# Kernel tuning notes

Hardware: AMD Instinct MI355X
Metric: run time of the kernel (lower is better)

The kernel has to match this reference:

```python
import jax, jax.numpy as jnp
import numpy as np

# SLAYER SRM-alpha neuron constants (standard slayerPytorch yaml defaults)
THETA = 10.0      # spike threshold
TAU_SR = 10.0     # synaptic response time constant
TAU_REF = 1.0     # refractory time constant
SCALE_REF = 2.0   # refractory scale (kernel amplitude = -scaleRef*theta)
TS = 1.0          # simulation timestep
K_LEN = 100       # SRM kernel truncation length (kernel is negligible beyond this)
A_REF = float(np.exp(-TS / TAU_REF))
# refractory alpha kernel ref[m] = K_REF * m * A_REF**m  (= -scaleRef*theta*(m*Ts/tauRef)*exp(1-m*Ts/tauRef))
K_REF = -SCALE_REF * THETA * float(np.e) * (TS / TAU_REF)


def _srm_kernel():
    # eps(t) = (t/tauSr) * exp(1 - t/tauSr), eps(0) = 0
    t = jnp.arange(K_LEN, dtype=jnp.float32) * TS
    return (t / TAU_SR) * jnp.exp(1.0 - t / TAU_SR)


def _psp(z):
    # z: (N, O, T). Causal FIR convolution in time with the SRM alpha kernel.
    N, O, T = z.shape
    k = _srm_kernel()[::-1].reshape(1, 1, K_LEN)  # flip: lax conv is correlation
    out = jax.lax.conv_general_dilated(z.reshape(N * O, 1, T), k,
                                       window_strides=(1,),
                                       padding=[(K_LEN - 1, 0)])
    return out.reshape(N, O, T)


def _refractory_and_spikes(u):
    # u: (T, N, O) post-synaptic potential. Sequential threshold + alpha refractory.
    # Alpha refractory kernel K*m*a^m is realized as a 2nd-order IIR over spikes:
    #   p[n] = a*p[n-1] + s[n]          (1st-order exp state)
    #   y[n] = a*(y[n-1] + K*p[n-1])    (refractory contribution at step n)
    def step(carry, u_t):
        p, y = carry
        y_n = A_REF * (y + K_REF * p)
        s = (u_t + y_n >= THETA).astype(u_t.dtype) / TS
        return (A_REF * p + s, y_n), (s, y_n)

    z0 = jnp.zeros(u.shape[1:], u.dtype)
    _, (s_seq, y_seq) = jax.lax.scan(step, (z0, z0), u)
    return s_seq, y_seq


def _layer(z):
    # slayer.spike(slayer.psp(fc(x)))
    u = _psp(z)
    s, _ = _refractory_and_spikes(jnp.moveaxis(u, -1, 0))
    return jnp.moveaxis(s, 0, -1)


def setup_inputs():
    key = jax.random.key(0)
    k1, k2, k3 = jax.random.split(key, 3)
    x = (jax.random.uniform(k1, (8, 2, 128, 128, 300)) < 0.03).astype(jnp.float32)
    # weight scales chosen so layer membranes hover around threshold -> realistic spiking
    w1 = jax.random.normal(k2, (410, 2 * 128 * 128), jnp.float32) * 0.01
    w2 = jax.random.normal(k3, (10, 410), jnp.float32) * 0.05
    return {"x": x, "w1": w1, "w2": w2}


def reference(x, w1, w2):
    N, T = x.shape[0], x.shape[-1]
    xf = x.reshape(N, -1, T)  # (N, C*H*W, T): slayer.dense is a full-spatial conv == GEMM per t
    s1 = _layer(jnp.einsum('nit,oi->not', xf, w1))  # fc1 -> psp -> spike, (N, 410, T)
    s2 = _layer(jnp.einsum('nit,oi->not', s1, w2))  # fc2 -> psp -> spike, (N, 10, T)
    return s2
```

## Files before the change

### kernel.cpp

```cpp
#include <hip/hip_runtime.h>

#define N_BATCH 8
#define I_DIM   32768
#define T_DIM   300
#define O1      410
#define O1P     416
#define O1Q     104
#define O2      10
#define KLEN    100
#define NCHUNK  16
#define NWORD   (I_DIM / 32)
#define CHCAP   128
#define NT      (N_BATCH * T_DIM)
#define GRP     4
#define NTG     (NT / GRP)
#define PSTRIDE 308

typedef float nfloat4 __attribute__((ext_vector_type(4)));

__device__ __forceinline__ float4 nt_load4(const float4* p) {
    nfloat4 v = __builtin_nontemporal_load(reinterpret_cast<const nfloat4*>(p));
    return make_float4(v.x, v.y, v.z, v.w);
}
__device__ __forceinline__ void nt_store4(float4* p, float4 v) {
    nfloat4 w = {v.x, v.y, v.z, v.w};
    __builtin_nontemporal_store(w, reinterpret_cast<nfloat4*>(p));
}

__global__ void transpose_w1_k(const float* __restrict__ w1, float* __restrict__ w1t) {
    __shared__ float tile[64][65];
    int i0 = blockIdx.x * 64;
    int o0 = blockIdx.y * 64;
    int tx = threadIdx.x & 63;
    int ty = threadIdx.x >> 6;
#pragma unroll
    for (int r = 0; r < 64; r += 4) {
        int o = o0 + r + ty;
        tile[r + ty][tx] = (o < O1) ? __builtin_nontemporal_load(&w1[(size_t)o * I_DIM + i0 + tx])
                                    : 0.0f;
    }
    __syncthreads();
#pragma unroll
    for (int r = 0; r < 64; r += 4) {
        int i = i0 + r + ty;
        int o = o0 + tx;
        if (o < O1P) w1t[(size_t)i * O1P + o] = (o < O1) ? tile[tx][r + ty] : 0.0f;
    }
}

__global__ __launch_bounds__(256) void bitmask_k(const float* __restrict__ x,
                                                 unsigned int* __restrict__ xb) {
    __shared__ float4 tile4[32 * 75];
    __shared__ unsigned int wbuf[300];
    int w   = blockIdx.x;
    int n   = blockIdx.y;
    int tid = threadIdx.x;
    const float4* src = (const float4*)(x + ((size_t)(n * I_DIM + w * 32)) * T_DIM);
    for (int q = tid; q < 32 * 75; q += 256) tile4[q] = nt_load4(&src[q]);
    __syncthreads();
    const float* tile = (const float*)tile4;
    int wv  = tid >> 6;
    int l   = tid & 63;
    int row = l & 31;
    int th  = l >> 5;
    for (int tp = wv; tp < 150; tp += 4) {
        int t = 2 * tp + th;
        float v = tile[row * 300 + t];
        unsigned long long m = __ballot(v != 0.0f);
        if (l == 0) {
            wbuf[2 * tp]     = (unsigned int)m;
            wbuf[2 * tp + 1] = (unsigned int)(m >> 32);
        }
    }
    __syncthreads();
    if (tid < 75) {
        uint4* dst = (uint4*)(xb + ((size_t)n * NWORD + w) * T_DIM);
        dst[tid] = ((const uint4*)wbuf)[tid];
    }
}

__device__ __forceinline__ void add4(float4& a, const float4 b) {
    a.x += b.x; a.y += b.y; a.z += b.z; a.w += b.w;
}

__global__ __launch_bounds__(512) void gather_partial_k(
        const float4* __restrict__ w1t4, const unsigned int* __restrict__ xb,
        float4* __restrict__ partial4) {
    int b     = blockIdx.x;
    int phase = b / (NTG * 8);
    int rem   = b - phase * (NTG * 8);
    int ntg   = rem >> 3;
    int k     = rem & 7;
    int chunk = phase * 8 + k;
    int nt0   = ntg * GRP;
    int tid   = threadIdx.x;
    int wv    = tid >> 6;
    int l     = tid & 63;

    __shared__ int s_idx[GRP][CHCAP];
    __shared__ int s_cnt[GRP];

    if ((wv & 1) == 0) {
        int g  = wv >> 1;
        int nt = nt0 + g;
        int n  = nt / T_DIM, t = nt - n * T_DIM;
        unsigned int word = xb[((size_t)n * NWORD + chunk * 64 + l) * T_DIM + t];
        int c   = __popc(word);
        int pfx = c;
#pragma unroll
        for (int d = 1; d < 64; d <<= 1) {
            int v = __shfl_up(pfx, d);
            if (l >= d) pfx += v;
        }
        pfx -= c;
        int base = chunk * 2048 + l * 32;
        while (word) {
            int bit = __ffs(word) - 1;
            if (pfx < CHCAP) s_idx[g][pfx] = base + bit;
            pfx++;
            word &= word - 1;
        }
        if (l == 63) s_cnt[g] = (pfx < CHCAP) ? pfx : CHCAP;
    }
    __syncthreads();

    int g  = tid >> 7;
    int oq = tid & 127;
    if (oq < O1Q) {
        const float4* wb = w1t4 + oq;
        int c = s_cnt[g];
        float4 z4 = make_float4(0.f, 0.f, 0.f, 0.f);
        float4 a0 = z4, a1 = z4, a2 = z4, a3 = z4;
        int j = 0;
        for (; j + 4 <= c; j += 4) {
            add4(a0, wb[(size_t)s_idx[g][j + 0] * O1Q]);
            add4(a1, wb[(size_t)s_idx[g][j + 1] * O1Q]);
            add4(a2, wb[(size_t)s_idx[g][j + 2] * O1Q]);
            add4(a3, wb[(size_t)s_idx[g][j + 3] * O1Q]);
        }
        for (; j < c; j++) add4(a0, wb[(size_t)s_idx[g][j] * O1Q]);
        add4(a0, a1); add4(a2, a3); add4(a0, a2);
        nt_store4(&partial4[((size_t)(nt0 + g) * NCHUNK + chunk) * O1Q + oq], a0);
    }
}

__global__ void reduce_k(const float* __restrict__ partial, float* __restrict__ up1) {
    int id = blockIdx.x * 256 + threadIdx.x;
    if (id >= NT * O1P) return;
    int nt = id / O1P;
    int o  = id - nt * O1P;
    const float* p = partial + (size_t)nt * NCHUNK * O1P + o;
    float s = 0.0f;
#pragma unroll
    for (int c = 0; c < NCHUNK; c++) s += __builtin_nontemporal_load(p + c * O1P);
    up1[id] = s;
}

__global__ __launch_bounds__(256) void psp_spike_k(const float* __restrict__ up,
                                                   float* __restrict__ s,
                                                   int OP, int O) {
    __shared__ float zrow[16 * PSTRIDE];
    __shared__ float urow[16 * PSTRIDE];
    __shared__ float kern[104];
    int o0  = blockIdx.x * 16;
    int n   = blockIdx.y;
    int tid = threadIdx.x;

    if (tid < 104) {
        float a = (float)tid / 10.0f;
        kern[tid] = (tid < KLEN) ? a * expf(1.0f - a) : 0.0f;
    }
    for (int idx = tid; idx < 16 * T_DIM; idx += 256) {
        int t = idx >> 4, o = idx & 15;
        zrow[o * PSTRIDE + t] = up[((size_t)n * T_DIM + t) * OP + o0 + o];
    }
    __syncthreads();
    for (int task = tid; task < 16 * 75; task += 256) {
        int o  = task & 15;
        int t0 = (task >> 4) * 4;
        const float* zr = &zrow[o * PSTRIDE];
        float v0 = zr[t0], v1 = zr[t0 + 1], v2 = zr[t0 + 2], v3 = zr[t0 + 3];
        float a0 = 0.f, a1 = 0.f, a2 = 0.f, a3 = 0.f;
        for (int m = 0; m < KLEN; m++) {
            float km = kern[m];
            a0 += km * v0; a1 += km * v1; a2 += km * v2; a3 += km * v3;
            v3 = v2; v2 = v1; v1 = v0;
            int j = t0 - m - 1;
            v0 = (j >= 0) ? zr[j] : 0.0f;
        }
        *reinterpret_cast<float4*>(&urow[o * PSTRIDE + t0]) = make_float4(a0, a1, a2, a3);
    }
    __syncthreads();
    if (tid < 16) {
        const float A = 0.36787944117144233f;
        const float K = -54.365636569180904f;
        float p = 0.0f, y = 0.0f;
        float* ur = &urow[tid * PSTRIDE];
        float* sr = &zrow[tid * PSTRIDE];
        for (int t0 = 0; t0 < 296; t0 += 8) {
            float4 ua = *(const float4*)&ur[t0];
            float4 ub = *(const float4*)&ur[t0 + 4];
            float uv[8] = {ua.x, ua.y, ua.z, ua.w, ub.x, ub.y, ub.z, ub.w};
            float sp[8];
#pragma unroll
            for (int q = 0; q < 8; q++) {
                y = A * (y + K * p);
                float v = (uv[q] + y >= 10.0f) ? 1.0f : 0.0f;
                p = A * p + v;
                sp[q] = v;
            }
            *(float4*)&sr[t0]     = make_float4(sp[0], sp[1], sp[2], sp[3]);
            *(float4*)&sr[t0 + 4] = make_float4(sp[4], sp[5], sp[6], sp[7]);
        }
        {
            float4 ua = *(const float4*)&ur[296];
            float uv[4] = {ua.x, ua.y, ua.z, ua.w};
            float sp[4];
#pragma unroll
            for (int q = 0; q < 4; q++) {
                y = A * (y + K * p);
                float v = (uv[q] + y >= 10.0f) ? 1.0f : 0.0f;
                p = A * p + v;
                sp[q] = v;
            }
            *(float4*)&sr[296] = make_float4(sp[0], sp[1], sp[2], sp[3]);
        }
    }
    __syncthreads();
    for (int task = tid; task < 16 * 75; task += 256) {
        int o = task & 15, q = task >> 4;
        int oo = o0 + o;
        if (oo < O) {
            float4 v = *(const float4*)&zrow[o * PSTRIDE + q * 4];
            *reinterpret_cast<float4*>(&s[((size_t)n * O + oo) * T_DIM + q * 4]) = v;
        }
    }
}

__global__ __launch_bounds__(256) void gemm2_k(const float* __restrict__ s1,
                                               const float* __restrict__ w2,
                                               float* __restrict__ up2) {
    __shared__ float w2s[O2 * O1];
    int tid = threadIdx.x;
    int nt  = blockIdx.x * 256 + tid;
    for (int q = tid; q < O2 * O1; q += 256) w2s[q] = w2[q];
    __syncthreads();
    if (nt >= NT) return;
    int n = nt / T_DIM, t = nt - n * T_DIM;
    float acc[O2];
#pragma unroll
    for (int k = 0; k < O2; k++) acc[k] = 0.0f;
    const float* sp = s1 + (size_t)n * O1 * T_DIM + t;
    for (int o = 0; o < O1; o++) {
        float v = sp[(size_t)o * T_DIM];
#pragma unroll
        for (int k = 0; k < O2; k++) acc[k] += w2s[k * O1 + o] * v;
    }
    float4* dst = (float4*)&up2[(size_t)nt * 16];
    dst[0] = make_float4(acc[0], acc[1], acc[2], acc[3]);
    dst[1] = make_float4(acc[4], acc[5], acc[6], acc[7]);
    dst[2] = make_float4(acc[8], acc[9], 0.f, 0.f);
    dst[3] = make_float4(0.f, 0.f, 0.f, 0.f);
}

extern "C" void kernel_launch(void* const* d_in, const int* in_sizes, int n_in,
                              void* d_out, int out_size, void* d_ws, size_t ws_size,
                              hipStream_t stream) {
    const float* x  = (const float*)d_in[0];
    const float* w1 = (const float*)d_in[1];
    const float* w2 = (const float*)d_in[2];
    float* out = (float*)d_out;

    char* ws = (char*)d_ws;
    float*        w1t     = (float*)ws;        ws += (size_t)I_DIM * O1P * 4;
    unsigned int* xb      = (unsigned int*)ws; ws += (size_t)N_BATCH * NWORD * T_DIM * 4;
    float*        partial = (float*)ws;        ws += (size_t)NT * NCHUNK * O1P * 4;
    float*        up1     = (float*)ws;        ws += (size_t)NT * O1P * 4;
    float*        s1      = (float*)ws;        ws += (size_t)N_BATCH * O1 * T_DIM * 4;
    float*        up2     = (float*)ws;

    transpose_w1_k<<<dim3(I_DIM / 64, (O1P + 63) / 64), 256, 0, stream>>>(w1, w1t);
    bitmask_k<<<dim3(NWORD, N_BATCH), 256, 0, stream>>>(x, xb);
    gather_partial_k<<<2 * NTG * 8, 512, 0, stream>>>((const float4*)w1t, xb,
                                                      (float4*)partial);
    reduce_k<<<(NT * O1P + 255) / 256, 256, 0, stream>>>(partial, up1);
    psp_spike_k<<<dim3((O1 + 15) / 16, N_BATCH), 256, 0, stream>>>(up1, s1, O1P, O1);
    gemm2_k<<<(NT + 255) / 256, 256, 0, stream>>>(s1, w2, up2);
    psp_spike_k<<<dim3(1, N_BATCH), 256, 0, stream>>>(up2, out, 16, O2);
}
```

Measured before the change: 367.0 us.

## Fuse prep kernels, split gather work by output half per wave, shrink gemm2 blocks

```diff
diff --git a/kernel.cpp b/kernel.cpp
--- a/kernel.cpp
+++ b/kernel.cpp
@@ -8,11 +8,11 @@
 #define O1Q     104
 #define O2      10
 #define KLEN    100
-#define NCHUNK  16
+#define NCH_I   16
 #define NWORD   (I_DIM / 32)
 #define CHCAP   128
 #define NT      (N_BATCH * T_DIM)
-#define GRP     4
+#define GRP     8
 #define NTG     (NT / GRP)
 #define PSTRIDE 308
 
@@ -27,55 +27,60 @@
     __builtin_nontemporal_store(w, reinterpret_cast<nfloat4*>(p));
 }
 
-__global__ void transpose_w1_k(const float* __restrict__ w1, float* __restrict__ w1t) {
-    __shared__ float tile[64][65];
-    int i0 = blockIdx.x * 64;
-    int o0 = blockIdx.y * 64;
-    int tx = threadIdx.x & 63;
-    int ty = threadIdx.x >> 6;
-#pragma unroll
-    for (int r = 0; r < 64; r += 4) {
-        int o = o0 + r + ty;
-        tile[r + ty][tx] = (o < O1) ? __builtin_nontemporal_load(&w1[(size_t)o * I_DIM + i0 + tx])
-                                    : 0.0f;
-    }
-    __syncthreads();
-#pragma unroll
-    for (int r = 0; r < 64; r += 4) {
-        int i = i0 + r + ty;
-        int o = o0 + tx;
-        if (o < O1P) w1t[(size_t)i * O1P + o] = (o < O1) ? tile[tx][r + ty] : 0.0f;
-    }
-}
-
-__global__ __launch_bounds__(256) void bitmask_k(const float* __restrict__ x,
-                                                 unsigned int* __restrict__ xb) {
-    __shared__ float4 tile4[32 * 75];
-    __shared__ unsigned int wbuf[300];
-    int w   = blockIdx.x;
-    int n   = blockIdx.y;
+__global__ __launch_bounds__(256) void prep_k(const float* __restrict__ x,
+                                              const float* __restrict__ w1,
+                                              unsigned int* __restrict__ xb,
+                                              float* __restrict__ w1t) {
+    __shared__ __attribute__((aligned(16))) char smem[39616];
+    int b   = blockIdx.x;
     int tid = threadIdx.x;
-    const float4* src = (const float4*)(x + ((size_t)(n * I_DIM + w * 32)) * T_DIM);
-    for (int q = tid; q < 32 * 75; q += 256) tile4[q] = nt_load4(&src[q]);
-    __syncthreads();
-    const float* tile = (const float*)tile4;
-    int wv  = tid >> 6;
-    int l   = tid & 63;
-    int row = l & 31;
-    int th  = l >> 5;
-    for (int tp = wv; tp < 150; tp += 4) {
-        int t = 2 * tp + th;
-        float v = tile[row * 300 + t];
-        unsigned long long m = __ballot(v != 0.0f);
-        if (l == 0) {
-            wbuf[2 * tp]     = (unsigned int)m;
-            wbuf[2 * tp + 1] = (unsigned int)(m >> 32);
-        }
-    }
-    __syncthreads();
-    if (tid < 75) {
-        uint4* dst = (uint4*)(xb + ((size_t)n * NWORD + w) * T_DIM);
-        dst[tid] = ((const uint4*)wbuf)[tid];
+    if (b < NWORD * N_BATCH) {
+        float4*       tile4 = (float4*)smem;
+        unsigned int* wbuf  = (unsigned int*)(smem + 38400);
+        int w = b & (NWORD - 1);
+        int n = b >> 10;
+        const float4* src = (const float4*)(x + ((size_t)(n * I_DIM + w * 32)) * T_DIM);
+        for (int q = tid; q < 32 * 75; q += 256) tile4[q] = nt_load4(&src[q]);
+        __syncthreads();
+        const float* tile = (const float*)tile4;
+        int wv  = tid >> 6;
+        int l   = tid & 63;
+        int row = l & 31;
+        int th  = l >> 5;
+        for (int tp = wv; tp < 150; tp += 4) {
+            int t = 2 * tp + th;
+            float v = tile[row * 300 + t];
+            unsigned long long m = __ballot(v != 0.0f);
+            if (l == 0) {
+                wbuf[2 * tp]     = (unsigned int)m;
+                wbuf[2 * tp + 1] = (unsigned int)(m >> 32);
+            }
+        }
+        __syncthreads();
+        if (tid < 75) {
+            uint4* dst = (uint4*)(xb + ((size_t)n * NWORD + w) * T_DIM);
+            dst[tid] = ((const uint4*)smem)[9600 / 4 * 0 + 38400 / 16 + tid];
+        }
+    } else {
+        float (*tile)[65] = reinterpret_cast<float(*)[65]>(smem);
+        int bb = b - NWORD * N_BATCH;
+        int i0 = (bb & 511) * 64;
+        int o0 = (bb >> 9) * 64;
+        int tx = tid & 63;
+        int ty = tid >> 6;
+#pragma unroll
+        for (int r = 0; r < 64; r += 4) {
+            int o = o0 + r + ty;
+            tile[r + ty][tx] = (o < O1)
+                ? __builtin_nontemporal_load(&w1[(size_t)o * I_DIM + i0 + tx]) : 0.0f;
+        }
+        __syncthreads();
+#pragma unroll
+        for (int r = 0; r < 64; r += 4) {
+            int i = i0 + r + ty;
+            int o = o0 + tx;
+            if (o < O1P) w1t[(size_t)i * O1P + o] = (o < O1) ? tile[tx][r + ty] : 0.0f;
+        }
     }
 }
 
@@ -91,56 +96,51 @@
     int rem   = b - phase * (NTG * 8);
     int ntg   = rem >> 3;
     int k     = rem & 7;
-    int chunk = phase * 8 + k;
-    int nt0   = ntg * GRP;
+    int combo = phase * 8 + k;
+    int ih    = combo >> 1;
+    int oh    = combo & 1;
     int tid   = threadIdx.x;
-    int wv    = tid >> 6;
+    int w     = tid >> 6;
     int l     = tid & 63;
 
     __shared__ int s_idx[GRP][CHCAP];
-    __shared__ int s_cnt[GRP];
-
-    if ((wv & 1) == 0) {
-        int g  = wv >> 1;
-        int nt = nt0 + g;
-        int n  = nt / T_DIM, t = nt - n * T_DIM;
-        unsigned int word = xb[((size_t)n * NWORD + chunk * 64 + l) * T_DIM + t];
-        int c   = __popc(word);
-        int pfx = c;
-#pragma unroll
-        for (int d = 1; d < 64; d <<= 1) {
-            int v = __shfl_up(pfx, d);
-            if (l >= d) pfx += v;
-        }
-        pfx -= c;
-        int base = chunk * 2048 + l * 32;
-        while (word) {
-            int bit = __ffs(word) - 1;
-            if (pfx < CHCAP) s_idx[g][pfx] = base + bit;
-            pfx++;
-            word &= word - 1;
-        }
-        if (l == 63) s_cnt[g] = (pfx < CHCAP) ? pfx : CHCAP;
-    }
-    __syncthreads();
-
-    int g  = tid >> 7;
-    int oq = tid & 127;
-    if (oq < O1Q) {
-        const float4* wb = w1t4 + oq;
-        int c = s_cnt[g];
+
+    int nt = ntg * GRP + w;
+    int n  = nt / T_DIM, t = nt - n * T_DIM;
+    unsigned int word = xb[((size_t)n * NWORD + ih * 64 + l) * T_DIM + t];
+    int c   = __popc(word);
+    int pfx = c;
+#pragma unroll
+    for (int d = 1; d < 64; d <<= 1) {
+        int v = __shfl_up(pfx, d);
+        if (l >= d) pfx += v;
+    }
+    int total = __shfl(pfx, 63);
+    if (total > CHCAP) total = CHCAP;
+    pfx -= c;
+    int base = ih * 2048 + l * 32;
+    while (word) {
+        int bit = __ffs(word) - 1;
+        if (pfx < CHCAP) s_idx[w][pfx] = base + bit;
+        pfx++;
+        word &= word - 1;
+    }
+
+    if (l < 52) {
+        const float4* wb = w1t4 + oh * 52 + l;
         float4 z4 = make_float4(0.f, 0.f, 0.f, 0.f);
         float4 a0 = z4, a1 = z4, a2 = z4, a3 = z4;
         int j = 0;
-        for (; j + 4 <= c; j += 4) {
-            add4(a0, wb[(size_t)s_idx[g][j + 0] * O1Q]);
-            add4(a1, wb[(size_t)s_idx[g][j + 1] * O1Q]);
-            add4(a2, wb[(size_t)s_idx[g][j + 2] * O1Q]);
-            add4(a3, wb[(size_t)s_idx[g][j + 3] * O1Q]);
-        }
-        for (; j < c; j++) add4(a0, wb[(size_t)s_idx[g][j] * O1Q]);
+        for (; j + 4 <= total; j += 4) {
+            int4 idx4 = *reinterpret_cast<const int4*>(&s_idx[w][j]);
+            add4(a0, wb[(size_t)idx4.x * O1Q]);
+            add4(a1, wb[(size_t)idx4.y * O1Q]);
+            add4(a2, wb[(size_t)idx4.z * O1Q]);
+            add4(a3, wb[(size_t)idx4.w * O1Q]);
+        }
+        for (; j < total; j++) add4(a0, wb[(size_t)s_idx[w][j] * O1Q]);
         add4(a0, a1); add4(a2, a3); add4(a0, a2);
-        nt_store4(&partial4[((size_t)(nt0 + g) * NCHUNK + chunk) * O1Q + oq], a0);
+        nt_store4(&partial4[((size_t)nt * NCH_I + ih) * O1Q + oh * 52 + l], a0);
     }
 }
 
@@ -149,10 +149,10 @@
     if (id >= NT * O1P) return;
     int nt = id / O1P;
     int o  = id - nt * O1P;
-    const float* p = partial + (size_t)nt * NCHUNK * O1P + o;
+    const float* p = partial + (size_t)nt * NCH_I * O1P + o;
     float s = 0.0f;
 #pragma unroll
-    for (int c = 0; c < NCHUNK; c++) s += __builtin_nontemporal_load(p + c * O1P);
+    for (int c = 0; c < NCH_I; c++) s += __builtin_nontemporal_load(p + c * O1P);
     up1[id] = s;
 }
 
@@ -237,13 +237,13 @@
     }
 }
 
-__global__ __launch_bounds__(256) void gemm2_k(const float* __restrict__ s1,
-                                               const float* __restrict__ w2,
-                                               float* __restrict__ up2) {
+__global__ __launch_bounds__(64) void gemm2_k(const float* __restrict__ s1,
+                                              const float* __restrict__ w2,
+                                              float* __restrict__ up2) {
     __shared__ float w2s[O2 * O1];
     int tid = threadIdx.x;
-    int nt  = blockIdx.x * 256 + tid;
-    for (int q = tid; q < O2 * O1; q += 256) w2s[q] = w2[q];
+    int nt  = blockIdx.x * 64 + tid;
+    for (int q = tid; q < O2 * O1; q += 64) w2s[q] = w2[q];
     __syncthreads();
     if (nt >= NT) return;
     int n = nt / T_DIM, t = nt - n * T_DIM;
@@ -274,17 +274,16 @@
     char* ws = (char*)d_ws;
     float*        w1t     = (float*)ws;        ws += (size_t)I_DIM * O1P * 4;
     unsigned int* xb      = (unsigned int*)ws; ws += (size_t)N_BATCH * NWORD * T_DIM * 4;
-    float*        partial = (float*)ws;        ws += (size_t)NT * NCHUNK * O1P * 4;
+    float*        partial = (float*)ws;        ws += (size_t)NT * NCH_I * O1P * 4;
     float*        up1     = (float*)ws;        ws += (size_t)NT * O1P * 4;
     float*        s1      = (float*)ws;        ws += (size_t)N_BATCH * O1 * T_DIM * 4;
     float*        up2     = (float*)ws;
 
-    transpose_w1_k<<<dim3(I_DIM / 64, (O1P + 63) / 64), 256, 0, stream>>>(w1, w1t);
-    bitmask_k<<<dim3(NWORD, N_BATCH), 256, 0, stream>>>(x, xb);
-    gather_partial_k<<<2 * NTG * 8, 512, 0, stream>>>((const float4*)w1t, xb,
+    prep_k<<<NWORD * N_BATCH + 512 * 7, 256, 0, stream>>>(x, w1, xb, w1t);
+    gather_partial_k<<<4 * NTG * 8, 512, 0, stream>>>((const float4*)w1t, xb,
                                                       (float4*)partial);
     reduce_k<<<(NT * O1P + 255) / 256, 256, 0, stream>>>(partial, up1);
     psp_spike_k<<<dim3((O1 + 15) / 16, N_BATCH), 256, 0, stream>>>(up1, s1, O1P, O1);
-    gemm2_k<<<(NT + 255) / 256, 256, 0, stream>>>(s1, w2, up2);
+    gemm2_k<<<(NT + 63) / 64, 64, 0, stream>>>(s1, w2, up2);
     psp_spike_k<<<dim3(1, N_BATCH), 256, 0, stream>>>(up2, out, 16, O2);
 }
```

Measured after the change: 378.8 us. 1.03x slower.
